# Performance work log

Measured on AMD Instinct MI355X. Metric: run time of the kernel, lower is better.

Reference implementation:

```python
import jax, jax.numpy as jnp
import numpy as np

N = 20000      # nodes
E = 320000     # edges
H = 256        # hidden_dim
BD = 64        # bond embedding dim
MSG_IN = 2 * H + BD  # 576


def setup_inputs() -> dict:
    key = jax.random.key(0)
    ks = jax.random.split(key, 24)
    s = 0.05
    inp = {}
    inp["x"] = jax.random.randint(ks[0], (N, 3), 0, 7).astype(jnp.float32)
    inp["edge_index"] = jax.random.randint(ks[1], (2, E), 0, N).astype(jnp.int32)
    inp["edge_attr"] = jax.random.randint(ks[2], (E, 1), 0, 5).astype(jnp.float32)
    inp["batch"] = jnp.zeros((N,), jnp.int32)
    # embedding tables
    inp["atom_table"] = jax.random.normal(ks[3], (11, 64), jnp.float32) * s
    inp["charge_table"] = jax.random.normal(ks[4], (7, 32), jnp.float32) * s
    inp["hybrid_table"] = jax.random.normal(ks[5], (8, 32), jnp.float32) * s
    inp["bond_table"] = jax.random.normal(ks[6], (5, BD), jnp.float32) * s
    # 3 stacked ChemicalGraphConv layers (weights stored [in, out])
    inp["gnn_w1"] = jax.random.normal(ks[7], (3, MSG_IN, H), jnp.float32) * s
    inp["gnn_b1"] = jnp.zeros((3, H), jnp.float32)
    inp["gnn_w2"] = jax.random.normal(ks[8], (3, H, H), jnp.float32) * s
    inp["gnn_b2"] = jnp.zeros((3, H), jnp.float32)
    inp["att_w"] = jax.random.normal(ks[9], (3, BD, 1), jnp.float32) * s
    inp["att_b"] = jnp.zeros((3, 1), jnp.float32)
    # chemical_properties MLP
    inp["prop_w1"] = jax.random.normal(ks[10], (H, 128), jnp.float32) * s
    inp["prop_b1"] = jnp.zeros((128,), jnp.float32)
    inp["prop_w2"] = jax.random.normal(ks[11], (128, 32), jnp.float32) * s
    inp["prop_b2"] = jnp.zeros((32,), jnp.float32)
    # 4 functional-group pattern encoders, stacked [4, H, 16]
    inp["fg_w"] = jax.random.normal(ks[12], (4, H, 16), jnp.float32) * s
    inp["fg_b"] = jnp.zeros((4, 16), jnp.float32)
    return inp


def reference(x, edge_index, edge_attr, batch,
              atom_table, charge_table, hybrid_table, bond_table,
              gnn_w1, gnn_b1, gnn_w2, gnn_b2, att_w, att_b,
              prop_w1, prop_b1, prop_w2, prop_b2, fg_w, fg_b):
    n = x.shape[0]
    atom_types = jnp.clip(x[:, 0].astype(jnp.int32), 0, 10)
    formal_charges = jnp.clip(x[:, 2].astype(jnp.int32) + 3, 0, 6)
    hybridization = jnp.clip(x[:, 1].astype(jnp.int32), 0, 7)
    bond_types = jnp.clip(edge_attr[:, 0].astype(jnp.int32), 0, 4)
    bond_emb = bond_table[bond_types]  # [E, 64]

    h = jnp.concatenate([atom_table[atom_types],
                         charge_table[formal_charges],
                         hybrid_table[hybridization]], axis=-1)  # [N, 128]
    h = jnp.pad(h, ((0, 0), (0, H - h.shape[1])))  # pad to hidden_dim

    row, col = edge_index[0], edge_index[1]
    for l in range(3):  # 3 ChemicalGraphConv layers
        gate = jax.nn.sigmoid(bond_emb @ att_w[l] + att_b[l])            # [E, 1]
        msg = jnp.concatenate([h[row], h[col], bond_emb], axis=-1)      # [E, 576]
        msg = jax.nn.relu(msg @ gnn_w1[l] + gnn_b1[l]) @ gnn_w2[l] + gnn_b2[l]
        msg = msg * gate                                                 # [E, H]
        h = h + jax.ops.segment_sum(msg, row, num_segments=n)

    chemical_props = jax.nn.relu(h @ prop_w1 + prop_b1) @ prop_w2 + prop_b2  # [N, 32]

    # FunctionalGroupDetector: mean(encoder(h)) == mean(h) @ W + b (linear)
    pooled = jnp.mean(h, axis=0)                                   # [H]
    fg = (jnp.einsum('d,kdo->ko', pooled, fg_w) + fg_b).reshape(-1)  # [64]
    fg_features = jnp.broadcast_to(fg, (n, 64))

    return h, chemical_props, fg_features, atom_types
```

## Files before the change

### kernel.cpp

```cpp
#include <hip/hip_runtime.h>
#include <stdint.h>

typedef unsigned short u16;
typedef unsigned int   u32;
typedef unsigned long long u64;
typedef __attribute__((ext_vector_type(8))) short bf16x8;
typedef __attribute__((ext_vector_type(4))) float f32x4;

#define NN 20000
#define NE 320000
#define HD 256
#define BD 64

#define WS_PRE   0u
#define WS_W1T   20480000u
#define WS_W2I   21266432u
#define WS_PW1   21659648u
#define WS_PW2   21725184u
#define WS_PREB  21733376u
#define WS_GATE  21748736u
#define WS_POOL  21748800u
#define WS_FGV   21749824u
#define WS_CNT   21750080u
#define WS_META  21830080u

__device__ __forceinline__ u16 f2bf(float f){
  u32 u = __float_as_uint(f);
  u += 0x7fffu + ((u >> 16) & 1u);
  return (u16)(u >> 16);
}
__device__ __forceinline__ u32 pk2(float a, float b){
  return (u32)f2bf(a) | ((u32)f2bf(b) << 16);
}
__device__ __forceinline__ float bf2f(u16 u){
  return __uint_as_float((u32)u << 16);
}
__device__ __forceinline__ u32 pk2t(float a, float b){
  return __builtin_amdgcn_perm(__float_as_uint(a), __float_as_uint(b), 0x03020706u);
}
__device__ __forceinline__ u32 relu_pack(u32 a, u32 b, float p0, float p1){
  float a0 = __uint_as_float(a << 16);
  float a1 = __uint_as_float(a & 0xffff0000u);
  float b0 = __uint_as_float(b << 16);
  float b1 = __uint_as_float(b & 0xffff0000u);
  float s0 = fmaxf(a0 + b0 + p0, 0.f);
  float s1 = fmaxf(a1 + b1 + p1, 0.f);
  return pk2t(s0, s1);
}
__device__ __forceinline__ void gl_lds16(const u16* g, u16* l){
  __builtin_amdgcn_global_load_lds(
      (const __attribute__((address_space(1))) unsigned int*)g,
      (__attribute__((address_space(3))) unsigned int*)l, 16, 0, 0);
}

__global__ void setup_k(const float* __restrict__ gw1,
                        const float* __restrict__ gw2,
                        const float* __restrict__ pw1,
                        const float* __restrict__ pw2,
                        const float* __restrict__ bond_table,
                        const float* __restrict__ gb1,
                        const float* __restrict__ att_w,
                        const float* __restrict__ att_b,
                        const float* __restrict__ x,
                        const float* __restrict__ atom_table,
                        const float* __restrict__ charge_table,
                        const float* __restrict__ hybrid_table,
                        u16* __restrict__ w1t, u16* __restrict__ w2img,
                        u16* __restrict__ pw1bf, u16* __restrict__ pw2bf,
                        float* __restrict__ preb,
                        float* __restrict__ gate_tab, float* __restrict__ pooled,
                        int* __restrict__ cnt,
                        float* __restrict__ h0, float* __restrict__ out_at){
  int i = blockIdx.x*256 + threadIdx.x;
  if (i < 442368){
    float v = gw1[i];
    int l = i / 147456;
    int r = i - l*147456;
    int srow = r >> 8, c = r & 255;
    if (srow < 512){
      int dc = (srow < 256) ? c : (256 + c);
      w1t[((size_t)l*512 + dc)*256 + (srow & 255)] = f2bf(v);
    }
  } else if (i < 638976){
    int t = i - 442368;
    float v = gw2[t];
    int l = t >> 16;
    int rest = t & 65535;
    int k = rest >> 8, c = rest & 255;
    int ks = k >> 5, k5 = k & 31;
    int kc = k5 >> 3, j = k5 & 7;
    int s = kc ^ ((c >> 1) & 3);
    w2img[(((l*8 + ks)*256 + c)*4 + s)*8 + j] = f2bf(v);
  } else if (i < 671744){
    int t = i - 638976;
    float v = pw1[t];
    int k = t >> 7, o = t & 127;
    pw1bf[o*256 + k] = f2bf(v);
  } else if (i < 675840){
    int t = i - 671744;
    float v = pw2[t];
    int k = t >> 5, o = t & 31;
    pw2bf[o*128 + k] = f2bf(v);
  } else if (i < 679680){
    int t = i - 675840;
    int l = t / 1280;
    int r = t - l*1280;
    int bt = r >> 8, c = r & 255;
    float s = gb1[l*HD + c];
    for (int d = 0; d < BD; ++d)
      s += bond_table[bt*BD + d] * gw1[(l*576 + 512 + d)*256 + c];
    preb[(l*5 + bt)*256 + c] = s;
  } else if (i < 679695){
    int t = i - 679680;
    int l = t / 5, b = t - 5*l;
    float s = att_b[l];
    for (int d = 0; d < BD; ++d) s += bond_table[b*BD + d] * att_w[l*BD + d];
    gate_tab[t] = 1.0f / (1.0f + __expf(-s));
  } else if (i < 679951){
    pooled[i - 679695] = 0.0f;
  } else if (i < 699951){
    cnt[i - 679951] = 0;
  } else if (i < 1339951){
    int t = i - 699951;
    int n = t >> 5, sub = t & 31, c0 = sub*8;
    int at = (int)x[n*3 + 0]; at = at < 0 ? 0 : (at > 10 ? 10 : at);
    float4 v0 = {0.f,0.f,0.f,0.f}, v1 = {0.f,0.f,0.f,0.f};
    if (c0 < 64){
      v0 = *(const float4*)(atom_table + at*64 + c0);
      v1 = *(const float4*)(atom_table + at*64 + c0 + 4);
    } else if (c0 < 96){
      int fc = (int)x[n*3 + 2] + 3; fc = fc < 0 ? 0 : (fc > 6 ? 6 : fc);
      v0 = *(const float4*)(charge_table + fc*32 + (c0 - 64));
      v1 = *(const float4*)(charge_table + fc*32 + (c0 - 64) + 4);
    } else if (c0 < 128){
      int hy = (int)x[n*3 + 1]; hy = hy < 0 ? 0 : (hy > 7 ? 7 : hy);
      v0 = *(const float4*)(hybrid_table + hy*32 + (c0 - 96));
      v1 = *(const float4*)(hybrid_table + hy*32 + (c0 - 96) + 4);
    }
    *(float4*)(h0 + (size_t)n*HD + c0)     = v0;
    *(float4*)(h0 + (size_t)n*HD + c0 + 4) = v1;
    if (sub == 0) out_at[n] = (float)at;
  }
}

__global__ void hist_k(const int* __restrict__ eidx, int* __restrict__ cnt){
  int e = blockIdx.x*256 + threadIdx.x;
  int r = eidx[e]; r = r < 0 ? 0 : (r >= NN ? NN-1 : r);
  atomicAdd(&cnt[r], 1);
}

__launch_bounds__(1024)
__global__ void scan_k(int* __restrict__ cnt){
  __shared__ int part[1024];
  int t = threadIdx.x;
  int base = t*20;
  int loc[20];
  int s = 0;
  #pragma unroll
  for (int j = 0; j < 20; ++j){
    int idx = base + j;
    int v = (idx < NN) ? cnt[idx] : 0;
    loc[j] = v; s += v;
  }
  part[t] = s; __syncthreads();
  for (int off = 1; off < 1024; off <<= 1){
    int v = (t >= off) ? part[t-off] : 0;
    __syncthreads();
    part[t] += v;
    __syncthreads();
  }
  int run = part[t] - s;
  #pragma unroll
  for (int j = 0; j < 20; ++j){
    int idx = base + j;
    if (idx < NN){ cnt[idx] = run; run += loc[j]; }
  }
}

__global__ void scatter_k(const int* __restrict__ eidx,
                          const float* __restrict__ eattr,
                          int* __restrict__ cur,
                          int2* __restrict__ smeta){
  int e = blockIdx.x*256 + threadIdx.x;
  int r = eidx[e];        r = r < 0 ? 0 : (r >= NN ? NN-1 : r);
  int c = eidx[NE + e];   c = c < 0 ? 0 : (c >= NN ? NN-1 : c);
  int bt = (int)eattr[e]; bt = bt < 0 ? 0 : (bt > 4 ? 4 : bt);
  int pos = atomicAdd(&cur[r], 1);
  if (pos >= 0 && pos < NE){
    int2 m; m.x = r | (bt << 20); m.y = c;
    smeta[pos] = m;
  }
}

__launch_bounds__(256, 4)
__global__ void pre_k(const float* __restrict__ h,
                      const u16* __restrict__ w1t,
                      u16* __restrict__ pre, int layer){
  __shared__ u16 a_lds[64*40];
  __shared__ u16 b_lds[256*40];
  const int tid = threadIdx.x;
  const int n0 = blockIdx.x * 64;
  const int half = blockIdx.y;
  const int w = tid >> 6, lane = tid & 63, g = lane >> 4, lr = lane & 15;
  const int rstage = tid >> 2, q = tid & 3;
  int arow = n0 + rstage; if (arow >= NN) arow = NN-1;
  const float* hrow = h + (size_t)arow*HD;
  const u16* bp = w1t + ((size_t)layer*512 + (size_t)half*256 + tid)*256;

  f32x4 acc[4][4];
  for (int mi = 0; mi < 4; ++mi)
    for (int nj = 0; nj < 4; ++nj)
      acc[mi][nj] = (f32x4){0.f,0.f,0.f,0.f};

  for (int ks = 0; ks < 8; ++ks){
    __syncthreads();
    {
      const float* src = hrow + ks*32 + q*8;
      float4 f0 = *(const float4*)src;
      float4 f1 = *(const float4*)(src + 4);
      uint4 av;
      av.x = pk2(f0.x,f0.y); av.y = pk2(f0.z,f0.w);
      av.z = pk2(f1.x,f1.y); av.w = pk2(f1.z,f1.w);
      *(uint4*)(a_lds + rstage*40 + q*8) = av;
    }
    {
      const u16* src = bp + ks*32;
      uint4 s0 = *(const uint4*)(src);
      uint4 s1 = *(const uint4*)(src + 8);
      uint4 s2 = *(const uint4*)(src + 16);
      uint4 s3 = *(const uint4*)(src + 24);
      u16* dst = b_lds + tid*40;
      *(uint4*)(dst)      = s0;
      *(uint4*)(dst + 8)  = s1;
      *(uint4*)(dst + 16) = s2;
      *(uint4*)(dst + 24) = s3;
    }
    __syncthreads();
    bf16x8 af[4], bfr[4];
    for (int mi = 0; mi < 4; ++mi)
      af[mi] = *(const bf16x8*)(a_lds + (mi*16 + lr)*40 + g*8);
    for (int nj = 0; nj < 4; ++nj)
      bfr[nj] = *(const bf16x8*)(b_lds + (w*64 + nj*16 + lr)*40 + g*8);
    for (int mi = 0; mi < 4; ++mi)
      for (int nj = 0; nj < 4; ++nj)
        acc[mi][nj] = __builtin_amdgcn_mfma_f32_16x16x32_bf16(af[mi], bfr[nj], acc[mi][nj], 0, 0, 0);
  }

  for (int mi = 0; mi < 4; ++mi)
    for (int nj = 0; nj < 4; ++nj)
      for (int p = 0; p < 4; ++p){
        int re = mi*16 + g*4 + p;
        int n = n0 + re;
        if (n < NN)
          pre[(size_t)n*512 + half*256 + w*64 + nj*16 + lr] = f2bf(acc[mi][nj][p]);
      }
}

__launch_bounds__(512, 4)
__global__ void edge_msg_k(const int2* __restrict__ smeta,
                           const u16* __restrict__ pre,
                           const float* __restrict__ prebg,
                           const u16* __restrict__ w2img,
                           const float* __restrict__ b2g,
                           const float* __restrict__ gate_tab,
                           float* __restrict__ h,
                           int layer){
  __shared__ u16 b_lds[16384];
  __shared__ u16 t_lds[64*264];
  __shared__ int   row_l[64];
  __shared__ float gate_l[64];
  __shared__ u64   mask_l;

  const int tid = threadIdx.x;
  const int bid = blockIdx.x;
  const int blk = (bid & 7)*625 + (bid >> 3);
  const int eBase = blk * 64;
  const int w = tid >> 6, lane = tid & 63, g = lane >> 4, lr = lane & 15;
  const int rstage = tid >> 3, q = tid & 7;

  const size_t wbase = (size_t)layer*65536;

  #pragma unroll
  for (int b = 0; b < 2; ++b)
    #pragma unroll
    for (int j = 0; j < 2; ++j)
      gl_lds16(w2img + wbase + (size_t)(b*256 + w*32 + j*16)*32 + lane*8,
               b_lds + b*8192 + w*1024 + j*512);

  int2 m0 = smeta[eBase + rstage];
  const int rI  = m0.x & 0xFFFFF;
  const int btI = (m0.x >> 20) & 7;
  const int cI  = m0.y;

  if (tid < 64){
    int2 mm = smeta[eBase + tid];
    int r = mm.x & 0xFFFFF;
    row_l[tid] = r;
    gate_l[tid] = gate_tab[layer*5 + ((mm.x >> 20) & 7)];
    int rprev = __shfl_up(r, 1);
    bool fl = (tid > 0) && (r != rprev);
    u64 mk = __ballot(fl);
    if (tid == 0) mask_l = mk;
  }

  {
    const u16* p1 = pre + (size_t)rI*512;
    const u16* p2 = pre + (size_t)cI*512 + 256;
    const float* pb = prebg + (size_t)(layer*5 + btI)*256;
    uint4 v1[4], v2[4];
    #pragma unroll
    for (int it = 0; it < 4; ++it){
      int c0 = it*64 + q*8;
      v1[it] = *(const uint4*)(p1 + c0);
      v2[it] = *(const uint4*)(p2 + c0);
    }
    #pragma unroll
    for (int it = 0; it < 4; ++it){
      int c0 = it*64 + q*8;
      float4 pa = *(const float4*)(pb + c0);
      float4 pc = *(const float4*)(pb + c0 + 4);
      uint4 ov;
      ov.x = relu_pack(v1[it].x, v2[it].x, pa.x, pa.y);
      ov.y = relu_pack(v1[it].y, v2[it].y, pa.z, pa.w);
      ov.z = relu_pack(v1[it].z, v2[it].z, pc.x, pc.y);
      ov.w = relu_pack(v1[it].w, v2[it].w, pc.z, pc.w);
      *(uint4*)(t_lds + rstage*264 + c0) = ov;
    }
  }

  __syncthreads();

  f32x4 acc[4][2];
  for (int mi = 0; mi < 4; ++mi)
    for (int nj = 0; nj < 2; ++nj)
      acc[mi][nj] = (f32x4){0.f,0.f,0.f,0.f};

  const int sw = (g ^ ((lr >> 1) & 3)) << 3;

  #pragma unroll
  for (int ks = 0; ks < 8; ++ks){
    if (ks >= 1 && ks < 7){
      #pragma unroll
      for (int j = 0; j < 2; ++j)
        gl_lds16(w2img + wbase + (size_t)((ks+1)*256 + w*32 + j*16)*32 + lane*8,
                 b_lds + ((ks+1)&1)*8192 + w*1024 + j*512);
      asm volatile("s_waitcnt vmcnt(2)" ::: "memory");
    } else if (ks == 0){
      asm volatile("s_waitcnt vmcnt(2)" ::: "memory");
    } else {
      asm volatile("s_waitcnt vmcnt(0)" ::: "memory");
    }
    const u16* bb = b_lds + (ks&1)*8192 + w*1024;
    bf16x8 af[4], bfr[2];
    for (int nj = 0; nj < 2; ++nj)
      bfr[nj] = *(const bf16x8*)(bb + (nj*16 + lr)*32 + sw);
    for (int mi = 0; mi < 4; ++mi)
      af[mi] = *(const bf16x8*)(t_lds + (mi*16 + lr)*264 + ks*32 + g*8);
    __builtin_amdgcn_s_setprio(1);
    for (int mi = 0; mi < 4; ++mi)
      for (int nj = 0; nj < 2; ++nj)
        acc[mi][nj] = __builtin_amdgcn_mfma_f32_16x16x32_bf16(af[mi], bfr[nj], acc[mi][nj], 0, 0, 0);
    __builtin_amdgcn_s_setprio(0);
  }

  {
    float b2v[2];
    for (int nj = 0; nj < 2; ++nj) b2v[nj] = b2g[layer*HD + w*32 + nj*16 + lr];
    for (int mi = 0; mi < 4; ++mi)
      for (int nj = 0; nj < 2; ++nj){
        u16* mb = b_lds + nj*8192 + w*1024 + lr*64;
        float v[4];
        #pragma unroll
        for (int p = 0; p < 4; ++p){
          int re = mi*16 + g*4 + p;
          v[p] = (acc[mi][nj][p] + b2v[nj]) * gate_l[re];
        }
        int slot = (mi*2 + (g >> 1)) ^ (lr & 7);
        uint2 pkv; pkv.x = pk2t(v[0], v[1]); pkv.y = pk2t(v[2], v[3]);
        *(uint2*)(mb + slot*8 + (g & 1)*4) = pkv;
      }
  }
  __syncthreads();

  {
    const int cl = tid & 255, half = tid >> 8;
    u64 mk = mask_l;
    u32 m32 = (u32)(mk >> (half ? 32 : 0));
    m32 = __builtin_amdgcn_readfirstlane(m32);
    const u16* mb = b_lds + ((cl >> 4) & 1)*8192 + (cl >> 5)*1024 + (cl & 15)*64;
    float run = 0.f;
    #pragma unroll
    for (int e8l = 0; e8l < 4; ++e8l){
      int e8 = half*4 + e8l;
      bf16x8 mv = *(const bf16x8*)(mb + ((e8 ^ (cl & 7)) << 3));
      #pragma unroll
      for (int j = 0; j < 8; ++j){
        int el = e8l*8 + j;
        run += bf2f((u16)mv[j]);
        bool fl = (el == 31) || ((m32 >> (el + 1)) & 1u);
        if (fl){
          int rr = row_l[half*32 + el];
          atomicAdd(h + (size_t)rr*HD + cl, run);
          run = 0.f;
        }
      }
    }
  }
}

__global__ void pool_k(const float* __restrict__ h,
                       float* __restrict__ pooled){
  int c = threadIdx.x;
  int r0 = blockIdx.x * 50;
  float s = 0.f;
  for (int r = r0; r < r0 + 50; ++r)
    s += h[(size_t)r*HD + c];
  atomicAdd(&pooled[c], s);
}

__global__ void fg_k(const float* __restrict__ pooled,
                     const float* __restrict__ fg_w,
                     const float* __restrict__ fg_b,
                     float* __restrict__ fg_vals){
  int o = threadIdx.x;
  int k = o >> 4, j = o & 15;
  float s = 0.f;
  for (int d = 0; d < HD; ++d) s += pooled[d] * fg_w[(size_t)k*HD*16 + d*16 + j];
  fg_vals[o] = s / (float)NN + fg_b[k*16 + j];
}

__global__ void bcast_fg_k(const float* __restrict__ fg_vals,
                           float* __restrict__ out_fg){
  __shared__ float fv[64];
  if (threadIdx.x < 64) fv[threadIdx.x] = fg_vals[threadIdx.x];
  __syncthreads();
  int i = blockIdx.x*256 + threadIdx.x;
  out_fg[i] = fv[i & 63];
}

__launch_bounds__(256, 3)
__global__ void props_mfma_k(const float* __restrict__ h,
                             const u16* __restrict__ pw1bf,
                             const float* __restrict__ pb1,
                             const u16* __restrict__ pw2bf,
                             const float* __restrict__ pb2,
                             float* __restrict__ outp){
  __shared__ u16 a_lds[64*40];
  __shared__ u16 b2_lds[128*40];
  __shared__ u16 t2[64*136];
  const int tid = threadIdx.x;
  const int n0 = blockIdx.x*64;
  const int w = tid >> 6, lane = tid & 63, g = lane >> 4, lr = lane & 15;
  const int rstage = tid >> 2, q = tid & 3;
  int arow = n0 + rstage; if (arow >= NN) arow = NN-1;
  const float* hrow = h + (size_t)arow*HD;

  const int colb = tid >> 1, halfb = tid & 1;

  f32x4 acc[4][2];
  for (int mi = 0; mi < 4; ++mi)
    for (int nj = 0; nj < 2; ++nj)
      acc[mi][nj] = (f32x4){0.f,0.f,0.f,0.f};

  for (int ks = 0; ks < 8; ++ks){
    __syncthreads();
    {
      const float* src = hrow + ks*32 + q*8;
      float4 f0 = *(const float4*)src;
      float4 f1 = *(const float4*)(src + 4);
      uint4 av;
      av.x = pk2(f0.x,f0.y); av.y = pk2(f0.z,f0.w);
      av.z = pk2(f1.x,f1.y); av.w = pk2(f1.z,f1.w);
      *(uint4*)(a_lds + rstage*40 + q*8) = av;
    }
    {
      const u16* src = pw1bf + colb*256 + ks*32 + halfb*16;
      uint4 s0 = *(const uint4*)src;
      uint4 s1 = *(const uint4*)(src + 8);
      u16* dst = b2_lds + colb*40 + halfb*16;
      *(uint4*)dst = s0; *(uint4*)(dst + 8) = s1;
    }
    __syncthreads();
    bf16x8 af[4], bfr[2];
    for (int mi = 0; mi < 4; ++mi)
      af[mi] = *(const bf16x8*)(a_lds + (mi*16 + lr)*40 + g*8);
    for (int nj = 0; nj < 2; ++nj)
      bfr[nj] = *(const bf16x8*)(b2_lds + (w*32 + nj*16 + lr)*40 + g*8);
    for (int mi = 0; mi < 4; ++mi)
      for (int nj = 0; nj < 2; ++nj)
        acc[mi][nj] = __builtin_amdgcn_mfma_f32_16x16x32_bf16(af[mi], bfr[nj], acc[mi][nj], 0, 0, 0);
  }

  {
    float b1v[2];
    for (int nj = 0; nj < 2; ++nj) b1v[nj] = pb1[w*32 + nj*16 + lr];
    for (int mi = 0; mi < 4; ++mi)
      for (int nj = 0; nj < 2; ++nj){
        int colt = w*32 + nj*16 + lr;
        for (int p = 0; p < 4; ++p){
          float v = acc[mi][nj][p] + b1v[nj];
          v = v > 0.f ? v : 0.f;
          t2[(mi*16 + g*4 + p)*136 + colt] = f2bf(v);
        }
      }
  }
  __syncthreads();

  {
    int col = tid >> 3, part = tid & 7;
    const u16* src = pw2bf + col*128 + part*16;
    u16* dst = b2_lds + col*136 + part*16;
    *(uint4*)dst       = *(const uint4*)src;
    *(uint4*)(dst + 8) = *(const uint4*)(src + 8);
  }
  __syncthreads();

  {
    f32x4 acc2[2];
    for (int nj = 0; nj < 2; ++nj) acc2[nj] = (f32x4){0.f,0.f,0.f,0.f};
    for (int ks = 0; ks < 4; ++ks){
      bf16x8 af = *(const bf16x8*)(t2 + (w*16 + lr)*136 + ks*32 + g*8);
      for (int nj = 0; nj < 2; ++nj){
        bf16x8 bf = *(const bf16x8*)(b2_lds + (nj*16 + lr)*136 + ks*32 + g*8);
        acc2[nj] = __builtin_amdgcn_mfma_f32_16x16x32_bf16(af, bf, acc2[nj], 0, 0, 0);
      }
    }
    for (int nj = 0; nj < 2; ++nj)
      for (int p = 0; p < 4; ++p){
        int n = n0 + w*16 + g*4 + p;
        int col = nj*16 + lr;
        if (n < NN)
          outp[(size_t)n*32 + col] = acc2[nj][p] + pb2[col];
      }
  }
}

extern "C" void kernel_launch(void* const* d_in, const int* in_sizes, int n_in,
                              void* d_out, int out_size, void* d_ws, size_t ws_size,
                              hipStream_t stream) {
  const float* x            = (const float*)d_in[0];
  const int*   eidx         = (const int*)  d_in[1];
  const float* eattr        = (const float*)d_in[2];
  const float* atom_table   = (const float*)d_in[4];
  const float* charge_table = (const float*)d_in[5];
  const float* hybrid_table = (const float*)d_in[6];
  const float* bond_table   = (const float*)d_in[7];
  const float* gw1          = (const float*)d_in[8];
  const float* gb1          = (const float*)d_in[9];
  const float* gw2          = (const float*)d_in[10];
  const float* gb2          = (const float*)d_in[11];
  const float* attw         = (const float*)d_in[12];
  const float* attb         = (const float*)d_in[13];
  const float* pw1          = (const float*)d_in[14];
  const float* pb1          = (const float*)d_in[15];
  const float* pw2          = (const float*)d_in[16];
  const float* pb2          = (const float*)d_in[17];
  const float* fgw          = (const float*)d_in[18];
  const float* fgb          = (const float*)d_in[19];

  float* out       = (float*)d_out;
  float* out_h     = out;
  float* out_props = out + (size_t)NN*HD;
  float* out_fg    = out_props + (size_t)NN*32;
  float* out_at    = out_fg + (size_t)NN*64;

  char* ws = (char*)d_ws;
  u16*   pre      = (u16*)  (ws + WS_PRE);
  u16*   w1t      = (u16*)  (ws + WS_W1T);
  u16*   w2img    = (u16*)  (ws + WS_W2I);
  u16*   pw1bf    = (u16*)  (ws + WS_PW1);
  u16*   pw2bf    = (u16*)  (ws + WS_PW2);
  float* prebg    = (float*)(ws + WS_PREB);
  float* gate_tab = (float*)(ws + WS_GATE);
  float* pooled   = (float*)(ws + WS_POOL);
  float* fg_vals  = (float*)(ws + WS_FGV);
  int*   cnt      = (int*)  (ws + WS_CNT);
  int2*  smeta    = (int2*) (ws + WS_META);

  setup_k<<<5235, 256, 0, stream>>>(gw1, gw2, pw1, pw2, bond_table, gb1, attw, attb,
                                    x, atom_table, charge_table, hybrid_table,
                                    w1t, w2img, pw1bf, pw2bf, prebg, gate_tab, pooled,
                                    cnt, out_h, out_at);

  hist_k<<<1250, 256, 0, stream>>>(eidx, cnt);
  scan_k<<<1, 1024, 0, stream>>>(cnt);
  scatter_k<<<1250, 256, 0, stream>>>(eidx, eattr, cnt, smeta);

  for (int l = 0; l < 3; ++l){
    pre_k<<<dim3(313, 2), 256, 0, stream>>>(out_h, w1t, pre, l);
    edge_msg_k<<<5000, 512, 0, stream>>>(smeta, pre, prebg, w2img,
                                         gb2, gate_tab, out_h, l);
  }

  pool_k<<<400, 256, 0, stream>>>(out_h, pooled);
  fg_k<<<1, 64, 0, stream>>>(pooled, fgw, fgb, fg_vals);
  props_mfma_k<<<313, 256, 0, stream>>>(out_h, pw1bf, pb1, pw2bf, pb2, out_props);
  bcast_fg_k<<<5000, 256, 0, stream>>>(fg_vals, out_fg);
}
```

Before: 377.9 us.

## Make edge message kernel persistent with W2 fragments held in registers

The edge message kernel now launches 512 persistent blocks, each looping over 9-10 edge tiles, instead of one block per 64-edge tile. Each wave loads its W2 slice once into registers as MFMA B fragments (from a plain transposed bf16 layout), so the per-tile global-to-LDS streaming and double buffering of W2 go away. This is meant to remove the repeated W2 reload per tile and the launch overhead. In exchange it uses many more registers (16 bf16x8 fragments per lane), which may lower occupancy, and tiles within a block no longer overlap their gather and compute phases.

```diff
diff --git a/kernel.cpp b/kernel.cpp
--- a/kernel.cpp
+++ b/kernel.cpp
@@ -14,7 +14,7 @@
 
 #define WS_PRE   0u
 #define WS_W1T   20480000u
-#define WS_W2I   21266432u
+#define WS_W2T   21266432u
 #define WS_PW1   21659648u
 #define WS_PW2   21725184u
 #define WS_PREB  21733376u
@@ -46,11 +46,6 @@
   float s0 = fmaxf(a0 + b0 + p0, 0.f);
   float s1 = fmaxf(a1 + b1 + p1, 0.f);
   return pk2t(s0, s1);
-}
-__device__ __forceinline__ void gl_lds16(const u16* g, u16* l){
-  __builtin_amdgcn_global_load_lds(
-      (const __attribute__((address_space(1))) unsigned int*)g,
-      (__attribute__((address_space(3))) unsigned int*)l, 16, 0, 0);
 }
 
 __global__ void setup_k(const float* __restrict__ gw1,
@@ -65,7 +60,7 @@
                         const float* __restrict__ atom_table,
                         const float* __restrict__ charge_table,
                         const float* __restrict__ hybrid_table,
-                        u16* __restrict__ w1t, u16* __restrict__ w2img,
+                        u16* __restrict__ w1t, u16* __restrict__ w2t,
                         u16* __restrict__ pw1bf, u16* __restrict__ pw2bf,
                         float* __restrict__ preb,
                         float* __restrict__ gate_tab, float* __restrict__ pooled,
@@ -85,12 +80,9 @@
     int t = i - 442368;
     float v = gw2[t];
     int l = t >> 16;
-    int rest = t & 65535;
-    int k = rest >> 8, c = rest & 255;
-    int ks = k >> 5, k5 = k & 31;
-    int kc = k5 >> 3, j = k5 & 7;
-    int s = kc ^ ((c >> 1) & 3);
-    w2img[(((l*8 + ks)*256 + c)*4 + s)*8 + j] = f2bf(v);
+    int k = (t >> 8) & 255;
+    int c = t & 255;
+    w2t[(((size_t)l*256 + c) << 8) | k] = f2bf(v);
   } else if (i < 671744){
     int t = i - 638976;
     float v = pw1[t];
@@ -260,148 +252,144 @@
 __global__ void edge_msg_k(const int2* __restrict__ smeta,
                            const u16* __restrict__ pre,
                            const float* __restrict__ prebg,
-                           const u16* __restrict__ w2img,
+                           const u16* __restrict__ w2t,
                            const float* __restrict__ b2g,
                            const float* __restrict__ gate_tab,
                            float* __restrict__ h,
                            int layer){
-  __shared__ u16 b_lds[16384];
   __shared__ u16 t_lds[64*264];
+  __shared__ u16 m_lds[16384];
   __shared__ int   row_l[64];
   __shared__ float gate_l[64];
   __shared__ u64   mask_l;
 
   const int tid = threadIdx.x;
-  const int bid = blockIdx.x;
-  const int blk = (bid & 7)*625 + (bid >> 3);
-  const int eBase = blk * 64;
   const int w = tid >> 6, lane = tid & 63, g = lane >> 4, lr = lane & 15;
   const int rstage = tid >> 3, q = tid & 7;
 
-  const size_t wbase = (size_t)layer*65536;
-
+  const u16* w2base = w2t + (size_t)layer*65536;
+  bf16x8 Bf[8][2];
   #pragma unroll
-  for (int b = 0; b < 2; ++b)
+  for (int ks = 0; ks < 8; ++ks)
     #pragma unroll
-    for (int j = 0; j < 2; ++j)
-      gl_lds16(w2img + wbase + (size_t)(b*256 + w*32 + j*16)*32 + lane*8,
-               b_lds + b*8192 + w*1024 + j*512);
-
-  int2 m0 = smeta[eBase + rstage];
-  const int rI  = m0.x & 0xFFFFF;
-  const int btI = (m0.x >> 20) & 7;
-  const int cI  = m0.y;
-
-  if (tid < 64){
-    int2 mm = smeta[eBase + tid];
-    int r = mm.x & 0xFFFFF;
-    row_l[tid] = r;
-    gate_l[tid] = gate_tab[layer*5 + ((mm.x >> 20) & 7)];
-    int rprev = __shfl_up(r, 1);
-    bool fl = (tid > 0) && (r != rprev);
-    u64 mk = __ballot(fl);
-    if (tid == 0) mask_l = mk;
-  }
-
-  {
-    const u16* p1 = pre + (size_t)rI*512;
-    const u16* p2 = pre + (size_t)cI*512 + 256;
-    const float* pb = prebg + (size_t)(layer*5 + btI)*256;
-    uint4 v1[4], v2[4];
-    #pragma unroll
-    for (int it = 0; it < 4; ++it){
-      int c0 = it*64 + q*8;
-      v1[it] = *(const uint4*)(p1 + c0);
-      v2[it] = *(const uint4*)(p2 + c0);
-    }
-    #pragma unroll
-    for (int it = 0; it < 4; ++it){
-      int c0 = it*64 + q*8;
-      float4 pa = *(const float4*)(pb + c0);
-      float4 pc = *(const float4*)(pb + c0 + 4);
-      uint4 ov;
-      ov.x = relu_pack(v1[it].x, v2[it].x, pa.x, pa.y);
-      ov.y = relu_pack(v1[it].y, v2[it].y, pa.z, pa.w);
-      ov.z = relu_pack(v1[it].z, v2[it].z, pc.x, pc.y);
-      ov.w = relu_pack(v1[it].w, v2[it].w, pc.z, pc.w);
-      *(uint4*)(t_lds + rstage*264 + c0) = ov;
-    }
-  }
-
-  __syncthreads();
-
-  f32x4 acc[4][2];
-  for (int mi = 0; mi < 4; ++mi)
     for (int nj = 0; nj < 2; ++nj)
-      acc[mi][nj] = (f32x4){0.f,0.f,0.f,0.f};
-
-  const int sw = (g ^ ((lr >> 1) & 3)) << 3;
-
+      Bf[ks][nj] = *(const bf16x8*)(w2base + (size_t)(w*32 + nj*16 + lr)*256 + ks*32 + g*8);
+
+  float b2v[2];
   #pragma unroll
-  for (int ks = 0; ks < 8; ++ks){
-    if (ks >= 1 && ks < 7){
+  for (int nj = 0; nj < 2; ++nj) b2v[nj] = b2g[layer*HD + w*32 + nj*16 + lr];
+
+  const int bidv = blockIdx.x;
+  const int xcd = bidv & 7, idx = bidv >> 3;
+  int tstart, tcnt;
+  if (idx < 49){ tstart = xcd*625 + idx*10;           tcnt = 10; }
+  else         { tstart = xcd*625 + 490 + (idx-49)*9; tcnt = 9;  }
+
+  for (int t = 0; t < tcnt; ++t){
+    const int eBase = (tstart + t)*64;
+    if (t) __syncthreads();
+
+    int2 m0 = smeta[eBase + rstage];
+    const int rI  = m0.x & 0xFFFFF;
+    const int btI = (m0.x >> 20) & 7;
+    const int cI  = m0.y;
+
+    if (tid < 64){
+      int2 mm = smeta[eBase + tid];
+      int r = mm.x & 0xFFFFF;
+      row_l[tid] = r;
+      gate_l[tid] = gate_tab[layer*5 + ((mm.x >> 20) & 7)];
+      int rprev = __shfl_up(r, 1);
+      bool fl = (tid > 0) && (r != rprev);
+      u64 mk = __ballot(fl);
+      if (tid == 0) mask_l = mk;
+    }
+
+    {
+      const u16* p1 = pre + (size_t)rI*512;
+      const u16* p2 = pre + (size_t)cI*512 + 256;
+      const float* pb = prebg + (size_t)(layer*5 + btI)*256;
+      uint4 v1[4], v2[4];
       #pragma unroll
-      for (int j = 0; j < 2; ++j)
-        gl_lds16(w2img + wbase + (size_t)((ks+1)*256 + w*32 + j*16)*32 + lane*8,
-                 b_lds + ((ks+1)&1)*8192 + w*1024 + j*512);
-      asm volatile("s_waitcnt vmcnt(2)" ::: "memory");
-    } else if (ks == 0){
-      asm volatile("s_waitcnt vmcnt(2)" ::: "memory");
-    } else {
-      asm volatile("s_waitcnt vmcnt(0)" ::: "memory");
-    }
-    const u16* bb = b_lds + (ks&1)*8192 + w*1024;
-    bf16x8 af[4], bfr[2];
-    for (int nj = 0; nj < 2; ++nj)
-      bfr[nj] = *(const bf16x8*)(bb + (nj*16 + lr)*32 + sw);
-    for (int mi = 0; mi < 4; ++mi)
-      af[mi] = *(const bf16x8*)(t_lds + (mi*16 + lr)*264 + ks*32 + g*8);
-    __builtin_amdgcn_s_setprio(1);
+      for (int it = 0; it < 4; ++it){
+        int c0 = it*64 + q*8;
+        v1[it] = *(const uint4*)(p1 + c0);
+        v2[it] = *(const uint4*)(p2 + c0);
+      }
+      #pragma unroll
+      for (int it = 0; it < 4; ++it){
+        int c0 = it*64 + q*8;
+        float4 pa = *(const float4*)(pb + c0);
+        float4 pc = *(const float4*)(pb + c0 + 4);
+        uint4 ov;
+        ov.x = relu_pack(v1[it].x, v2[it].x, pa.x, pa.y);
+        ov.y = relu_pack(v1[it].y, v2[it].y, pa.z, pa.w);
+        ov.z = relu_pack(v1[it].z, v2[it].z, pc.x, pc.y);
+        ov.w = relu_pack(v1[it].w, v2[it].w, pc.z, pc.w);
+        *(uint4*)(t_lds + rstage*264 + c0) = ov;
+      }
+    }
+
+    __syncthreads();
+
+    f32x4 acc[4][2];
     for (int mi = 0; mi < 4; ++mi)
       for (int nj = 0; nj < 2; ++nj)
-        acc[mi][nj] = __builtin_amdgcn_mfma_f32_16x16x32_bf16(af[mi], bfr[nj], acc[mi][nj], 0, 0, 0);
-    __builtin_amdgcn_s_setprio(0);
-  }
-
-  {
-    float b2v[2];
-    for (int nj = 0; nj < 2; ++nj) b2v[nj] = b2g[layer*HD + w*32 + nj*16 + lr];
-    for (int mi = 0; mi < 4; ++mi)
-      for (int nj = 0; nj < 2; ++nj){
-        u16* mb = b_lds + nj*8192 + w*1024 + lr*64;
-        float v[4];
+        acc[mi][nj] = (f32x4){0.f,0.f,0.f,0.f};
+
+    #pragma unroll
+    for (int ks = 0; ks < 8; ++ks){
+      bf16x8 af[4];
+      #pragma unroll
+      for (int mi = 0; mi < 4; ++mi)
+        af[mi] = *(const bf16x8*)(t_lds + (mi*16 + lr)*264 + ks*32 + g*8);
+      __builtin_amdgcn_s_setprio(1);
+      #pragma unroll
+      for (int mi = 0; mi < 4; ++mi){
+        acc[mi][0] = __builtin_amdgcn_mfma_f32_16x16x32_bf16(af[mi], Bf[ks][0], acc[mi][0], 0, 0, 0);
+        acc[mi][1] = __builtin_amdgcn_mfma_f32_16x16x32_bf16(af[mi], Bf[ks][1], acc[mi][1], 0, 0, 0);
+      }
+      __builtin_amdgcn_s_setprio(0);
+    }
+
+    {
+      for (int mi = 0; mi < 4; ++mi)
+        for (int nj = 0; nj < 2; ++nj){
+          u16* mb = m_lds + nj*8192 + w*1024 + lr*64;
+          float v[4];
+          #pragma unroll
+          for (int p = 0; p < 4; ++p){
+            int re = mi*16 + g*4 + p;
+            v[p] = (acc[mi][nj][p] + b2v[nj]) * gate_l[re];
+          }
+          int slot = (mi*2 + (g >> 1)) ^ (lr & 7);
+          uint2 pkv; pkv.x = pk2t(v[0], v[1]); pkv.y = pk2t(v[2], v[3]);
+          *(uint2*)(mb + slot*8 + (g & 1)*4) = pkv;
+        }
+    }
+    __syncthreads();
+
+    {
+      const int cl = tid & 255, half = tid >> 8;
+      u64 mk = mask_l;
+      u32 m32 = (u32)(mk >> (half ? 32 : 0));
+      m32 = __builtin_amdgcn_readfirstlane(m32);
+      const u16* mb = m_lds + ((cl >> 4) & 1)*8192 + (cl >> 5)*1024 + (cl & 15)*64;
+      float run = 0.f;
+      #pragma unroll
+      for (int e8l = 0; e8l < 4; ++e8l){
+        int e8 = half*4 + e8l;
+        bf16x8 mv = *(const bf16x8*)(mb + ((e8 ^ (cl & 7)) << 3));
         #pragma unroll
-        for (int p = 0; p < 4; ++p){
-          int re = mi*16 + g*4 + p;
-          v[p] = (acc[mi][nj][p] + b2v[nj]) * gate_l[re];
-        }
-        int slot = (mi*2 + (g >> 1)) ^ (lr & 7);
-        uint2 pkv; pkv.x = pk2t(v[0], v[1]); pkv.y = pk2t(v[2], v[3]);
-        *(uint2*)(mb + slot*8 + (g & 1)*4) = pkv;
-      }
-  }
-  __syncthreads();
-
-  {
-    const int cl = tid & 255, half = tid >> 8;
-    u64 mk = mask_l;
-    u32 m32 = (u32)(mk >> (half ? 32 : 0));
-    m32 = __builtin_amdgcn_readfirstlane(m32);
-    const u16* mb = b_lds + ((cl >> 4) & 1)*8192 + (cl >> 5)*1024 + (cl & 15)*64;
-    float run = 0.f;
-    #pragma unroll
-    for (int e8l = 0; e8l < 4; ++e8l){
-      int e8 = half*4 + e8l;
-      bf16x8 mv = *(const bf16x8*)(mb + ((e8 ^ (cl & 7)) << 3));
-      #pragma unroll
-      for (int j = 0; j < 8; ++j){
-        int el = e8l*8 + j;
-        run += bf2f((u16)mv[j]);
-        bool fl = (el == 31) || ((m32 >> (el + 1)) & 1u);
-        if (fl){
-          int rr = row_l[half*32 + el];
-          atomicAdd(h + (size_t)rr*HD + cl, run);
-          run = 0.f;
+        for (int j = 0; j < 8; ++j){
+          int el = e8l*8 + j;
+          run += bf2f((u16)mv[j]);
+          bool fl = (el == 31) || ((m32 >> (el + 1)) & 1u);
+          if (fl){
+            int rr = row_l[half*32 + el];
+            atomicAdd(h + (size_t)rr*HD + cl, run);
+            run = 0.f;
+          }
         }
       }
     }
@@ -567,7 +555,7 @@
   char* ws = (char*)d_ws;
   u16*   pre      = (u16*)  (ws + WS_PRE);
   u16*   w1t      = (u16*)  (ws + WS_W1T);
-  u16*   w2img    = (u16*)  (ws + WS_W2I);
+  u16*   w2t      = (u16*)  (ws + WS_W2T);
   u16*   pw1bf    = (u16*)  (ws + WS_PW1);
   u16*   pw2bf    = (u16*)  (ws + WS_PW2);
   float* prebg    = (float*)(ws + WS_PREB);
@@ -579,7 +567,7 @@
 
   setup_k<<<5235, 256, 0, stream>>>(gw1, gw2, pw1, pw2, bond_table, gb1, attw, attb,
                                     x, atom_table, charge_table, hybrid_table,
-                                    w1t, w2img, pw1bf, pw2bf, prebg, gate_tab, pooled,
+                                    w1t, w2t, pw1bf, pw2bf, prebg, gate_tab, pooled,
                                     cnt, out_h, out_at);
 
   hist_k<<<1250, 256, 0, stream>>>(eidx, cnt);
@@ -588,8 +576,8 @@
 
   for (int l = 0; l < 3; ++l){
     pre_k<<<dim3(313, 2), 256, 0, stream>>>(out_h, w1t, pre, l);
-    edge_msg_k<<<5000, 512, 0, stream>>>(smeta, pre, prebg, w2img,
-                                         gb2, gate_tab, out_h, l);
+    edge_msg_k<<<512, 512, 0, stream>>>(smeta, pre, prebg, w2t,
+                                        gb2, gate_tab, out_h, l);
   }
 
   pool_k<<<400, 256, 0, stream>>>(out_h, pooled);
```

Measured after the change: 461.2 us. 22.0% more time.
